# Kernel tuning notes

Hardware: AMD Instinct MI355X
Metric: run time of the kernel (lower is better)

Reference implementation:

```python
import jax, jax.numpy as jnp
import numpy as np

D_MODEL = 2048
N_HEAD = 16
B, T = 2, 2048
D_HEAD = D_MODEL // N_HEAD          # 128
D_Q = D_MODEL // 3                  # 682
D_KV = D_MODEL // 2                 # 1024
D_QK_N = D_HEAD // 2                # 64
D_QK_R = D_HEAD // 2                # 64
LN_EPS = 1e-5


def setup_inputs() -> dict:
    key = jax.random.key(0)
    ks = jax.random.split(key, 8)
    s = 0.02
    return {
        'x': jax.random.normal(ks[0], (B, T, D_MODEL), dtype=jnp.float32),
        'Wdq_w': jax.random.normal(ks[1], (D_Q, D_MODEL), dtype=jnp.float32) * s,
        'Wdq_b': jnp.zeros((D_Q,), jnp.float32),
        'qn_g': jnp.ones((D_Q,), jnp.float32),
        'qn_b': jnp.zeros((D_Q,), jnp.float32),
        'Wuq_w': jax.random.normal(ks[2], (D_MODEL, D_Q), dtype=jnp.float32) * s,
        'Wuq_b': jnp.zeros((D_MODEL,), jnp.float32),
        'Wdkv_w': jax.random.normal(ks[3], (D_KV + D_QK_R, D_MODEL), dtype=jnp.float32) * s,
        'Wdkv_b': jnp.zeros((D_KV + D_QK_R,), jnp.float32),
        'kvn_g': jnp.ones((D_KV,), jnp.float32),
        'kvn_b': jnp.zeros((D_KV,), jnp.float32),
        'Wukv_w': jax.random.normal(ks[4], (D_MODEL + N_HEAD * D_QK_N, D_KV), dtype=jnp.float32) * s,
        'Wukv_b': jnp.zeros((D_MODEL + N_HEAD * D_QK_N,), jnp.float32),
        'Wo_w': jax.random.normal(ks[5], (D_MODEL, D_MODEL), dtype=jnp.float32) * s,
        'Wo_b': jnp.zeros((D_MODEL,), jnp.float32),
    }


def _linear(x, w, b):
    return jnp.einsum('...i,oi->...o', x, w) + b


def _layernorm(x, g, b):
    mu = jnp.mean(x, axis=-1, keepdims=True)
    var = jnp.mean(jnp.square(x - mu), axis=-1, keepdims=True)
    return (x - mu) * jax.lax.rsqrt(var + LN_EPS) * g + b


def _rotary(x):
    # Faithful to source: positions are taken from axis 1 of x (B, A, T, d)
    A, d = x.shape[1], x.shape[-1]
    inv_freq = (1.0 / 10000.0) ** (jnp.arange(0, d, 2, dtype=jnp.float32) / d)
    freqs = jnp.arange(A, dtype=jnp.float32)[:, None] * inv_freq[None, :]
    cos = jnp.cos(freqs)[None, :, None, :]
    sin = jnp.sin(freqs)[None, :, None, :]
    x1, x2 = jnp.split(x, 2, axis=-1)
    return jnp.concatenate([x1 * cos + x2 * sin, -x1 * sin + x2 * cos], axis=-1)


def reference(x, Wdq_w, Wdq_b, qn_g, qn_b, Wuq_w, Wuq_b,
              Wdkv_w, Wdkv_b, kvn_g, kvn_b, Wukv_w, Wukv_b, Wo_w, Wo_b):
    Bx, Tx, C = x.shape
    # Q path: down-proj -> norm -> up-proj
    c_q = _layernorm(_linear(x, Wdq_w, Wdq_b), qn_g, qn_b)
    q = _linear(c_q, Wuq_w, Wuq_b).reshape(Bx, Tx, N_HEAD, D_HEAD).transpose(0, 2, 1, 3)
    q_n, q_r = q[..., :D_QK_N], q[..., D_QK_N:]
    q_r = _rotary(q_r)
    # KV path
    c_kv = _linear(x, Wdkv_w, Wdkv_b)
    kv_n, k_r = c_kv[..., :D_KV], c_kv[..., D_KV:]
    kv_n = _layernorm(kv_n, kvn_g, kvn_b)
    kv = _linear(kv_n, Wukv_w, Wukv_b).reshape(Bx, Tx, N_HEAD, D_HEAD + D_QK_N).transpose(0, 2, 1, 3)
    k_n, v = kv[..., :D_QK_N], kv[..., D_QK_N:]
    k_r = k_r.reshape(Bx, Tx, 1, D_QK_R).transpose(0, 2, 1, 3)  # (B,1,T,dr)
    k_r = _rotary(k_r)  # identity here (single position), kept for fidelity
    k_r = jnp.broadcast_to(k_r, (Bx, N_HEAD, Tx, D_QK_R))
    q_full = jnp.concatenate([q_n, q_r], axis=-1)   # (B,H,T,d_head)
    k_full = jnp.concatenate([k_n, k_r], axis=-1)   # (B,H,T,d_head)
    # causal SDPA (scale = 1/sqrt(q dim))
    scale = 1.0 / np.sqrt(D_HEAD)
    scores = jnp.einsum('bhqd,bhkd->bhqk', q_full, k_full) * scale
    causal = jnp.tril(jnp.ones((Tx, Tx), dtype=bool))
    scores = jnp.where(causal[None, None], scores, jnp.finfo(scores.dtype).min)
    p = jax.nn.softmax(scores, axis=-1)
    y = jnp.einsum('bhqk,bhkd->bhqd', p, v)
    y = y.transpose(0, 2, 1, 3).reshape(Bx, Tx, C)
    return _linear(y, Wo_w, Wo_b)
```

## Files before the change

### kernel.cpp

```cpp
#include <hip/hip_runtime.h>
#include <math.h>

#define TOK 4096
#define DM 2048
#define DQ 682
#define DQP 704
#define DKV 1024
#define DUKV 3072
#define NH 16
#define T_SEQ 2048
#define NQKV 1792

typedef __attribute__((ext_vector_type(8))) short short8;
typedef __attribute__((ext_vector_type(4))) float floatx4;
typedef __attribute__((ext_vector_type(2))) unsigned int uint2v;

__device__ __forceinline__ unsigned short f2bf(float f) {
  union { float f; unsigned int u; } v; v.f = f;
  unsigned int u = v.u;
  u += 0x7fffu + ((u >> 16) & 1u);
  return (unsigned short)(u >> 16);
}
__device__ __forceinline__ unsigned short f2bf_fast(float f) {
  union { float f; unsigned int u; } v; v.f = f;
  return (unsigned short)((v.u + 0x8000u) >> 16);
}

typedef __attribute__((address_space(1))) const unsigned int as1_u32;
typedef __attribute__((address_space(3))) unsigned int as3_u32;
__device__ __forceinline__ void async16(const void* g, void* l) {
  __builtin_amdgcn_global_load_lds((as1_u32*)g, (as3_u32*)l, 16, 0, 0);
}

__global__ __launch_bounds__(256) void gemm_bf16_db(
    const unsigned short* __restrict__ A, int lda,
    const unsigned short* __restrict__ B, int ldb,
    const float* __restrict__ bias, float* __restrict__ C, int ldc,
    int Nvalid, int K)
{
  __shared__ __align__(16) unsigned short sm[16384];
  const int tid = threadIdx.x;
  const int w = tid >> 6;
  const int lane = tid & 63;
  const int q = lane >> 4;
  const int r = lane & 15;
  const int bm = blockIdx.y * 128;
  const int bn = blockIdx.x * 128;

  floatx4 acc[4][4];
#pragma unroll
  for (int i = 0; i < 4; i++)
#pragma unroll
    for (int j = 0; j < 4; j++) acc[i][j] = (floatx4){0.f, 0.f, 0.f, 0.f};

  const int srow = tid >> 2;
  const int scol = (tid & 3) * 8;
  const unsigned short* Ag0 = A + (size_t)(bm + srow) * lda + scol;
  const unsigned short* Ag1 = A + (size_t)(bm + 64 + srow) * lda + scol;
  const unsigned short* Bg0 = B + (size_t)(bn + srow) * ldb + scol;
  const unsigned short* Bg1 = B + (size_t)(bn + 64 + srow) * ldb + scol;

  const int mrow0 = (w >> 1) * 64;
  const int ncol0 = (w & 1) * 64;

  async16(Ag0, &sm[w * 512]);
  async16(Ag1, &sm[2048 + w * 512]);
  async16(Bg0, &sm[8192 + w * 512]);
  async16(Bg1, &sm[8192 + 2048 + w * 512]);

  for (int k0 = 0; k0 < K; k0 += 32) {
    const int cur = (k0 >> 5) & 1;
    __syncthreads();
    if (k0 + 32 < K) {
      const int nxt = cur ^ 1;
      async16(Ag0 + k0 + 32, &sm[nxt * 4096 + w * 512]);
      async16(Ag1 + k0 + 32, &sm[nxt * 4096 + 2048 + w * 512]);
      async16(Bg0 + k0 + 32, &sm[8192 + nxt * 4096 + w * 512]);
      async16(Bg1 + k0 + 32, &sm[8192 + nxt * 4096 + 2048 + w * 512]);
    }
    const unsigned short* As = &sm[cur * 4096];
    const unsigned short* Bs = &sm[8192 + cur * 4096];
    short8 a[4], b[4];
#pragma unroll
    for (int i = 0; i < 4; i++)
      a[i] = *(const short8*)&As[(mrow0 + i * 16 + r) * 32 + q * 8];
#pragma unroll
    for (int j = 0; j < 4; j++)
      b[j] = *(const short8*)&Bs[(ncol0 + j * 16 + r) * 32 + q * 8];
#pragma unroll
    for (int i = 0; i < 4; i++)
#pragma unroll
      for (int j = 0; j < 4; j++)
        acc[i][j] = __builtin_amdgcn_mfma_f32_16x16x32_bf16(a[i], b[j], acc[i][j], 0, 0, 0);
  }

#pragma unroll
  for (int j = 0; j < 4; j++) {
    int gc = bn + ncol0 + j * 16 + r;
    if (gc >= Nvalid) continue;
    float bv = bias[gc];
#pragma unroll
    for (int i = 0; i < 4; i++) {
#pragma unroll
      for (int v = 0; v < 4; v++) {
        int gr = bm + mrow0 + i * 16 + q * 4 + v;
        C[(size_t)gr * ldc + gc] = acc[i][j][v] + bv;
      }
    }
  }
}

__global__ __launch_bounds__(256) void gemm_up_fused(
    const unsigned short* __restrict__ Aq, const unsigned short* __restrict__ Bq,
    const float* __restrict__ biasq, unsigned short* __restrict__ Qall,
    const unsigned short* __restrict__ Akv, const unsigned short* __restrict__ Bkv,
    const float* __restrict__ biaskv, unsigned short* __restrict__ kvout)
{
  __shared__ __align__(16) unsigned short sm[16384];
  const int tid = threadIdx.x;
  const int w = tid >> 6;
  const int lane = tid & 63;
  const int q = lane >> 4;
  const int r = lane & 15;
  const int bx = blockIdx.x;
  const bool isQ = bx < 16;
  const int bn = isQ ? bx * 128 : (bx - 16) * 128;
  const int bm = blockIdx.y * 128;
  const int K = isQ ? DQP : DKV;
  const unsigned short* A = isQ ? Aq : Akv;
  const unsigned short* B = isQ ? Bq : Bkv;

  floatx4 acc[4][4];
#pragma unroll
  for (int i = 0; i < 4; i++)
#pragma unroll
    for (int j = 0; j < 4; j++) acc[i][j] = (floatx4){0.f, 0.f, 0.f, 0.f};

  const int srow = tid >> 2;
  const int scol = (tid & 3) * 8;
  const unsigned short* Ag0 = A + (size_t)(bm + srow) * K + scol;
  const unsigned short* Ag1 = A + (size_t)(bm + 64 + srow) * K + scol;
  const unsigned short* Bg0 = B + (size_t)(bn + srow) * K + scol;
  const unsigned short* Bg1 = B + (size_t)(bn + 64 + srow) * K + scol;

  const int mrow0 = (w >> 1) * 64;
  const int ncol0 = (w & 1) * 64;

  async16(Ag0, &sm[w * 512]);
  async16(Ag1, &sm[2048 + w * 512]);
  async16(Bg0, &sm[8192 + w * 512]);
  async16(Bg1, &sm[8192 + 2048 + w * 512]);

  for (int k0 = 0; k0 < K; k0 += 32) {
    const int cur = (k0 >> 5) & 1;
    __syncthreads();
    if (k0 + 32 < K) {
      const int nxt = cur ^ 1;
      async16(Ag0 + k0 + 32, &sm[nxt * 4096 + w * 512]);
      async16(Ag1 + k0 + 32, &sm[nxt * 4096 + 2048 + w * 512]);
      async16(Bg0 + k0 + 32, &sm[8192 + nxt * 4096 + w * 512]);
      async16(Bg1 + k0 + 32, &sm[8192 + nxt * 4096 + 2048 + w * 512]);
    }
    const unsigned short* As = &sm[cur * 4096];
    const unsigned short* Bs = &sm[8192 + cur * 4096];
    short8 a[4], b[4];
#pragma unroll
    for (int i = 0; i < 4; i++)
      a[i] = *(const short8*)&As[(mrow0 + i * 16 + r) * 32 + q * 8];
#pragma unroll
    for (int j = 0; j < 4; j++)
      b[j] = *(const short8*)&Bs[(ncol0 + j * 16 + r) * 32 + q * 8];
#pragma unroll
    for (int i = 0; i < 4; i++)
#pragma unroll
      for (int j = 0; j < 4; j++)
        acc[i][j] = __builtin_amdgcn_mfma_f32_16x16x32_bf16(a[i], b[j], acc[i][j], 0, 0, 0);
  }

  if (!isQ) {
#pragma unroll
    for (int j = 0; j < 4; j++) {
      int gc = bn + ncol0 + j * 16 + r;
      float bv = biaskv[gc];
#pragma unroll
      for (int i = 0; i < 4; i++) {
#pragma unroll
        for (int v = 0; v < 4; v++) {
          int gr = bm + mrow0 + i * 16 + q * 4 + v;
          kvout[(size_t)gr * DUKV + gc] = f2bf(acc[i][j][v] + bv);
        }
      }
    }
    return;
  }

  const int h = bx;
  const float QS = (float)(0.08838834764831845 * 1.4426950408889634);
  if ((w & 1) == 0) {
#pragma unroll
    for (int j = 0; j < 4; j++) {
      int d = j * 16 + r;
      float bv = biasq[h * 128 + d];
#pragma unroll
      for (int i = 0; i < 4; i++) {
#pragma unroll
        for (int v = 0; v < 4; v++) {
          int gr = bm + mrow0 + i * 16 + q * 4 + v;
          int bb = gr >> 11, t = gr & 2047;
          Qall[(((size_t)(bb * NH + h)) * T_SEQ + t) * 128 + d] =
              f2bf((acc[i][j][v] + bv) * QS);
        }
      }
    }
  } else {
    float cs[2], sn[2], bv1[2], bv2[2];
#pragma unroll
    for (int jp = 0; jp < 2; jp++) {
      int jj = jp * 16 + r;
      float ang = (float)h * exp2f(-(float)jj * (13.287712379549449f / 32.0f));
      cs[jp] = cosf(ang); sn[jp] = sinf(ang);
      bv1[jp] = biasq[h * 128 + 64 + jj];
      bv2[jp] = biasq[h * 128 + 96 + jj];
    }
#pragma unroll
    for (int i = 0; i < 4; i++) {
#pragma unroll
      for (int v = 0; v < 4; v++) {
        int gr = bm + mrow0 + i * 16 + q * 4 + v;
        int bb = gr >> 11, t = gr & 2047;
        unsigned short* Qr = Qall + (((size_t)(bb * NH + h)) * T_SEQ + t) * 128;
#pragma unroll
        for (int jp = 0; jp < 2; jp++) {
          int jj = jp * 16 + r;
          float x1 = acc[i][jp][v] + bv1[jp];
          float x2 = acc[i][jp + 2][v] + bv2[jp];
          Qr[64 + jj] = f2bf((x1 * cs[jp] + x2 * sn[jp]) * QS);
          Qr[96 + jj] = f2bf((x2 * cs[jp] - x1 * sn[jp]) * QS);
        }
      }
    }
  }
}

__global__ __launch_bounds__(256) void cvt_bf16_pad(
    const float* __restrict__ in, unsigned short* __restrict__ out,
    int irows, int icols, int ocols, long total)
{
  long idx = (long)blockIdx.x * 256 + threadIdx.x;
  if (idx >= total) return;
  int rr = (int)(idx / ocols);
  int cc = (int)(idx - (long)rr * ocols);
  out[idx] = (rr < irows && cc < icols) ? f2bf(in[(size_t)rr * icols + cc]) : 0;
}

__device__ __forceinline__ void cvt_region(
    const float* __restrict__ in, unsigned short* __restrict__ out,
    int irows, int icols, int ocols, long idx)
{
  int rr = (int)(idx / ocols);
  int cc = (int)(idx - (long)rr * ocols);
  out[idx] = (rr < irows && cc < icols) ? f2bf(in[(size_t)rr * icols + cc]) : 0;
}

__global__ __launch_bounds__(256) void prep_weights(
    const float* __restrict__ Wdq_w, const float* __restrict__ Wdkv_w,
    const float* __restrict__ Wuq_w, const float* __restrict__ Wukv_w,
    const float* __restrict__ Wo_w,
    const float* __restrict__ Wdq_b, const float* __restrict__ Wdkv_b,
    unsigned short* __restrict__ Wqkv_bf, unsigned short* __restrict__ Wuq_bf,
    unsigned short* __restrict__ Wukv_bf, unsigned short* __restrict__ Wo_bf,
    float* __restrict__ bias_qkv)
{
  const long bx = blockIdx.x;
  if (bx < 5632) {
    cvt_region(Wdq_w, Wqkv_bf, 682, 2048, 2048, bx * 256 + threadIdx.x);
  } else if (bx < 14336) {
    cvt_region(Wdkv_w, Wqkv_bf + 704L * 2048, 1088, 2048, 2048,
               (bx - 5632) * 256 + threadIdx.x);
  } else if (bx < 19968) {
    cvt_region(Wuq_w, Wuq_bf, 2048, 682, 704, (bx - 14336) * 256 + threadIdx.x);
  } else if (bx < 32256) {
    cvt_region(Wukv_w, Wukv_bf, 3072, 1024, 1024, (bx - 19968) * 256 + threadIdx.x);
  } else if (bx < 48640) {
    cvt_region(Wo_w, Wo_bf, 2048, 2048, 2048, (bx - 32256) * 256 + threadIdx.x);
  } else {
    int i = (int)(bx - 48640) * 256 + threadIdx.x;
    if (i < NQKV)
      bias_qkv[i] = (i < DQ) ? Wdq_b[i] : ((i < DQP) ? 0.f : Wdkv_b[i - DQP]);
  }
}

__device__ __forceinline__ float block_sum(float v, float* sbuf) {
#pragma unroll
  for (int off = 32; off > 0; off >>= 1) v += __shfl_down(v, off, 64);
  int wid = threadIdx.x >> 6;
  __syncthreads();
  if ((threadIdx.x & 63) == 0) sbuf[wid] = v;
  __syncthreads();
  return sbuf[0] + sbuf[1] + sbuf[2] + sbuf[3];
}

__global__ __launch_bounds__(256) void ln_bf16_kernel(
    const float* __restrict__ in, int istride,
    unsigned short* __restrict__ out, int ocols,
    const float* __restrict__ g, const float* __restrict__ bta, int D)
{
  __shared__ float sbuf[4];
  size_t row = blockIdx.x;
  const float* xr = in + row * istride;
  float s = 0.f;
  for (int i = threadIdx.x; i < D; i += 256) s += xr[i];
  float mu = block_sum(s, sbuf) / (float)D;
  float v = 0.f;
  for (int i = threadIdx.x; i < D; i += 256) { float d = xr[i] - mu; v += d * d; }
  float var = block_sum(v, sbuf) / (float)D;
  float rstd = rsqrtf(var + 1e-5f);
  unsigned short* orow = out + row * ocols;
  for (int i = threadIdx.x; i < ocols; i += 256)
    orow[i] = (i < D) ? f2bf((xr[i] - mu) * rstd * g[i] + bta[i]) : 0;
}

__global__ __launch_bounds__(256) void repack_k_blk(
    const unsigned short* __restrict__ kv_bf, const float* __restrict__ cqkv,
    unsigned short* __restrict__ K)
{
  int idx = blockIdx.x * 256 + threadIdx.x;
  int dlow = idx & 31;
  int tt   = (idx >> 5) & 63;
  int dhi  = (idx >> 11) & 3;
  int kt   = (idx >> 13) & 31;
  int bh   = idx >> 18;
  int d = dhi * 32 + dlow;
  int t = kt * 64 + tt;
  int b = bh >> 4, h = bh & 15;
  unsigned short val;
  if (d < 64)
    val = kv_bf[((size_t)(b * T_SEQ + t)) * DUKV + h * 192 + d];
  else
    val = f2bf(cqkv[((size_t)(b * T_SEQ + t)) * NQKV + 1728 + (d - 64)]);
  K[idx] = val;
}

__global__ __launch_bounds__(256) void repack_v_blk(
    const unsigned short* __restrict__ kv_bf, unsigned short* __restrict__ V)
{
  __shared__ unsigned short T[64 * 132];
  int kt = blockIdx.x, bh = blockIdx.y;
  int b = bh >> 4, h = bh & 15;
  int tid = threadIdx.x;
#pragma unroll
  for (int p = 0; p < 8; p++) {
    int t = p * 8 + (tid >> 5);
    int dbase = (tid & 31) * 4;
    const unsigned short* src =
        kv_bf + ((size_t)(b * T_SEQ + kt * 64 + t)) * DUKV + h * 192 + 64 + dbase;
    unsigned short v0 = src[0], v1 = src[1], v2 = src[2], v3 = src[3];
    unsigned short* dst = &T[t * 132 + dbase];
    dst[0] = v0; dst[1] = v1; dst[2] = v2; dst[3] = v3;
  }
  __syncthreads();
  unsigned short* out = V + ((size_t)(bh * 32 + kt)) * 8192;
#pragma unroll
  for (int p = 0; p < 4; p++) {
    int o = p * 2048 + tid * 8;
    int c2 = o >> 12;
    int dd = (o >> 5) & 127;
    int tl = o & 31;
    short8 pack;
#pragma unroll
    for (int i = 0; i < 8; i++)
      pack[i] = (short)T[(c2 * 32 + tl + i) * 132 + dd];
    *(short8*)&out[o] = pack;
  }
}

__global__ __launch_bounds__(256, 2) void attn_mfma3(
    const unsigned short* __restrict__ Qall,
    const unsigned short* __restrict__ Kblk,
    const unsigned short* __restrict__ Vblk,
    unsigned short* __restrict__ y)
{
  __shared__ __align__(16) unsigned short sm[37376];
  const int x = (int)blockIdx.x;
  const int b = (int)blockIdx.z;
  const int qt = b ? (15 - x) : x;
  const int h = blockIdx.y;
  const int tid = threadIdx.x;
  const int w = tid >> 6, lane = tid & 63, q = lane >> 4, r = lane & 15;
  const int bh = b * NH + h;

  short8 qb[2][4];
#pragma unroll
  for (int g = 0; g < 2; g++) {
    const unsigned short* Qrow =
        Qall + ((size_t)bh * T_SEQ + (size_t)qt * 128 + w * 32 + g * 16 + r) * 128 + q * 8;
#pragma unroll
    for (int c = 0; c < 4; c++) qb[g][c] = *(const short8*)(Qrow + c * 32);
  }

  floatx4 oacc[2][8];
#pragma unroll
  for (int g = 0; g < 2; g++)
#pragma unroll
    for (int jd = 0; jd < 8; jd++) oacc[g][jd] = (floatx4){0.f, 0.f, 0.f, 0.f};
  float m_i[2] = {-3.0e38f, -3.0e38f}, l_i[2] = {0.f, 0.f};

  const char* Kg0 = (const char*)(Kblk + ((size_t)(bh * 32)) * 8192);
  const char* Vg0 = (const char*)(Vblk + ((size_t)(bh * 32)) * 8192);
  char* smB = (char*)sm;
  unsigned short* Psw = sm + 32768 + w * 1152;
  const int ktmax = 2 * qt + 1;

#pragma unroll
  for (int i = 0; i < 4; i++) {
    async16(Kg0 + i * 4096 + w * 1024 + lane * 16, smB + i * 4096 + w * 1024);
    async16(Vg0 + i * 4096 + w * 1024 + lane * 16, smB + 32768 + i * 4096 + w * 1024);
  }

  for (int kt = 0; kt <= ktmax; kt++) {
    const int cur = kt & 1;
    __syncthreads();
    if (kt < ktmax) {
      const int nxt = cur ^ 1;
      const char* Kg = Kg0 + (size_t)(kt + 1) * 16384;
      const char* Vg = Vg0 + (size_t)(kt + 1) * 16384;
#pragma unroll
      for (int i = 0; i < 4; i++) {
        async16(Kg + i * 4096 + w * 1024 + lane * 16,
                smB + nxt * 16384 + i * 4096 + w * 1024);
        async16(Vg + i * 4096 + w * 1024 + lane * 16,
                smB + 32768 + nxt * 16384 + i * 4096 + w * 1024);
      }
    }

    const bool activeW = (kt * 64 <= qt * 128 + w * 32 + 31);
    if (activeW) {
      const unsigned short* KsC = sm + cur * 8192;
      const unsigned short* VsC = sm + 16384 + cur * 8192;

      floatx4 sacc[2][4];
#pragma unroll
      for (int g = 0; g < 2; g++)
#pragma unroll
        for (int j = 0; j < 4; j++) sacc[g][j] = (floatx4){0.f, 0.f, 0.f, 0.f};
#pragma unroll
      for (int c = 0; c < 4; c++) {
        short8 ak[4];
#pragma unroll
        for (int j = 0; j < 4; j++)
          ak[j] = *(const short8*)&KsC[c * 2048 + (j * 16 + r) * 32 + q * 8];
#pragma unroll
        for (int g = 0; g < 2; g++)
#pragma unroll
          for (int j = 0; j < 4; j++)
            sacc[g][j] = __builtin_amdgcn_mfma_f32_16x16x32_bf16(ak[j], qb[g][c], sacc[g][j], 0, 0, 0);
      }

#pragma unroll
      for (int g = 0; g < 2; g++) {
        float sv[16];
#pragma unroll
        for (int j = 0; j < 4; j++)
#pragma unroll
          for (int v = 0; v < 4; v++) sv[j * 4 + v] = sacc[g][j][v];
        const int rel = qt * 128 + w * 32 + g * 16 + r - kt * 64;
        if (rel < 63) {
#pragma unroll
          for (int j = 0; j < 4; j++)
#pragma unroll
            for (int v = 0; v < 4; v++)
              if (j * 16 + q * 4 + v > rel) sv[j * 4 + v] = -3.0e38f;
        }
        float rm = sv[0];
#pragma unroll
        for (int t16 = 1; t16 < 16; t16++) rm = fmaxf(rm, sv[t16]);
        rm = fmaxf(rm, __shfl_xor(rm, 16, 64));
        rm = fmaxf(rm, __shfl_xor(rm, 32, 64));
        float mnew = fmaxf(m_i[g], rm);
        float alpha = exp2f(m_i[g] - mnew);
        m_i[g] = mnew;
        float p[16], rsum = 0.f;
#pragma unroll
        for (int t16 = 0; t16 < 16; t16++) { p[t16] = exp2f(sv[t16] - mnew); rsum += p[t16]; }
        rsum += __shfl_xor(rsum, 16, 64);
        rsum += __shfl_xor(rsum, 32, 64);
        l_i[g] = l_i[g] * alpha + rsum;
#pragma unroll
        for (int jd = 0; jd < 8; jd++) {
          oacc[g][jd][0] *= alpha; oacc[g][jd][1] *= alpha;
          oacc[g][jd][2] *= alpha; oacc[g][jd][3] *= alpha;
        }
#pragma unroll
        for (int j = 0; j < 4; j++) {
          unsigned int lo = (unsigned int)f2bf_fast(p[j * 4 + 0]) |
                            ((unsigned int)f2bf_fast(p[j * 4 + 1]) << 16);
          unsigned int hi = (unsigned int)f2bf_fast(p[j * 4 + 2]) |
                            ((unsigned int)f2bf_fast(p[j * 4 + 3]) << 16);
          uint2v pk; pk[0] = lo; pk[1] = hi;
          *(uint2v*)&Psw[r * 72 + j * 16 + q * 4] = pk;
        }
#pragma unroll
        for (int c2 = 0; c2 < 2; c2++) {
          short8 pb = *(const short8*)&Psw[r * 72 + c2 * 32 + q * 8];
#pragma unroll
          for (int jd = 0; jd < 8; jd++) {
            short8 bv = *(const short8*)&VsC[c2 * 4096 + (jd * 16 + r) * 32 + q * 8];
            oacc[g][jd] = __builtin_amdgcn_mfma_f32_16x16x32_bf16(bv, pb, oacc[g][jd], 0, 0, 0);
          }
        }
      }
    }
  }

#pragma unroll
  for (int g = 0; g < 2; g++) {
    float inv = 1.0f / l_i[g];
    unsigned short* yr =
        y + ((size_t)(b * T_SEQ) + (size_t)qt * 128 + w * 32 + g * 16 + r) * DM + h * 128;
#pragma unroll
    for (int jd = 0; jd < 8; jd++) {
      unsigned short o0 = f2bf(oacc[g][jd][0] * inv);
      unsigned short o1 = f2bf(oacc[g][jd][1] * inv);
      unsigned short o2 = f2bf(oacc[g][jd][2] * inv);
      unsigned short o3 = f2bf(oacc[g][jd][3] * inv);
      unsigned int lo = (unsigned int)o0 | ((unsigned int)o1 << 16);
      unsigned int hi = (unsigned int)o2 | ((unsigned int)o3 << 16);
      unsigned int* dst = (unsigned int*)(yr + jd * 16 + q * 4);
      dst[0] = lo; dst[1] = hi;
    }
  }
}

extern "C" void kernel_launch(void* const* d_in, const int* in_sizes, int n_in,
                              void* d_out, int out_size, void* d_ws, size_t ws_size,
                              hipStream_t stream) {
  const float* x      = (const float*)d_in[0];
  const float* Wdq_w  = (const float*)d_in[1];
  const float* Wdq_b  = (const float*)d_in[2];
  const float* qn_g   = (const float*)d_in[3];
  const float* qn_b   = (const float*)d_in[4];
  const float* Wuq_w  = (const float*)d_in[5];
  const float* Wuq_b  = (const float*)d_in[6];
  const float* Wdkv_w = (const float*)d_in[7];
  const float* Wdkv_b = (const float*)d_in[8];
  const float* kvn_g  = (const float*)d_in[9];
  const float* kvn_b  = (const float*)d_in[10];
  const float* Wukv_w = (const float*)d_in[11];
  const float* Wukv_b = (const float*)d_in[12];
  const float* Wo_w   = (const float*)d_in[13];
  const float* Wo_b   = (const float*)d_in[14];
  float* out = (float*)d_out;

  float* ws = (float*)d_ws;
  unsigned short* x_bf    = (unsigned short*)(ws);
  unsigned short* y_bf    = (unsigned short*)(ws);
  unsigned short* Wqkv_bf = (unsigned short*)(ws + 4194304);
  unsigned short* Wuq_bf  = (unsigned short*)(ws + 6029312);
  unsigned short* Wukv_bf = (unsigned short*)(ws + 6750208);
  float* bias_qkv = ws + 8323072;
  float* c_qkv    = ws + 8324864;
  unsigned short* c_q_bf = (unsigned short*)(ws + 15664896);
  unsigned short* kvn_bf = (unsigned short*)(ws + 17106688);
  unsigned short* kv_bf  = (unsigned short*)(ws + 19203840);
  unsigned short* Q_all  = (unsigned short*)(ws + 25495296);
  unsigned short* K_blk  = (unsigned short*)(ws + 29689600);
  unsigned short* V_blk  = (unsigned short*)(ws + 33883904);
  unsigned short* Wo_bf  = (unsigned short*)(ws + 38078208);

  dim3 blk(256);

  cvt_bf16_pad<<<(4096L*2048 + 255) / 256, blk, 0, stream>>>(x, x_bf, 4096, 2048, 2048, 4096L*2048);
  prep_weights<<<48647, blk, 0, stream>>>(Wdq_w, Wdkv_w, Wuq_w, Wukv_w, Wo_w,
                                          Wdq_b, Wdkv_b,
                                          Wqkv_bf, Wuq_bf, Wukv_bf, Wo_bf, bias_qkv);

  gemm_bf16_db<<<dim3(14, 32), blk, 0, stream>>>(x_bf, 2048, Wqkv_bf, 2048, bias_qkv, c_qkv, NQKV, NQKV, 2048);
  ln_bf16_kernel<<<TOK, blk, 0, stream>>>(c_qkv, NQKV, c_q_bf, DQP, qn_g, qn_b, DQ);
  ln_bf16_kernel<<<TOK, blk, 0, stream>>>(c_qkv + DQP, NQKV, kvn_bf, DKV, kvn_g, kvn_b, DKV);
  gemm_up_fused<<<dim3(40, 32), blk, 0, stream>>>(c_q_bf, Wuq_bf, Wuq_b, Q_all,
                                                  kvn_bf, Wukv_bf, Wukv_b, kv_bf);
  repack_k_blk<<<(2 * NH * T_SEQ * 128) / 256, blk, 0, stream>>>(kv_bf, c_qkv, K_blk);
  repack_v_blk<<<dim3(32, 32), blk, 0, stream>>>(kv_bf, V_blk);
  attn_mfma3<<<dim3(16, 16, 2), blk, 0, stream>>>(Q_all, K_blk, V_blk, y_bf);
  gemm_bf16_db<<<dim3(16, 32), blk, 0, stream>>>(y_bf, 2048, Wo_bf, 2048, Wo_b, out, DM, DM, 2048);
}
```

Before: 426.9 us.

## Fuse K/V repacking into GEMM epilogues and share rope keys across heads

The up-projection epilogue now writes K_nope and V straight into the blocked attention layouts, so the kv_bf buffer and the two repack kernels go away. The down-projection GEMM writes the rope key once per batch in blocked bf16 form, and attention loads it from a buffer shared by all heads. The two layernorm launches become one dual kernel, and the attention grid is flattened so causal tiles are scheduled in a new order. The scattered 2-byte epilogue stores are uncoalesced and could cost more than the repack passes they replace.

```diff
diff --git a/kernel.cpp b/kernel.cpp
--- a/kernel.cpp
+++ b/kernel.cpp
@@ -110,11 +110,98 @@
   }
 }
 
+__global__ __launch_bounds__(256) void gemm_dqkv(
+    const unsigned short* __restrict__ A,
+    const unsigned short* __restrict__ B,
+    const float* __restrict__ bias, float* __restrict__ C,
+    unsigned short* __restrict__ Kr)
+{
+  __shared__ __align__(16) unsigned short sm[16384];
+  const int tid = threadIdx.x;
+  const int w = tid >> 6;
+  const int lane = tid & 63;
+  const int q = lane >> 4;
+  const int r = lane & 15;
+  const int bm = blockIdx.y * 128;
+  const int bn = blockIdx.x * 128;
+  const int K = 2048;
+
+  floatx4 acc[4][4];
+#pragma unroll
+  for (int i = 0; i < 4; i++)
+#pragma unroll
+    for (int j = 0; j < 4; j++) acc[i][j] = (floatx4){0.f, 0.f, 0.f, 0.f};
+
+  const int srow = tid >> 2;
+  const int scol = (tid & 3) * 8;
+  const unsigned short* Ag0 = A + (size_t)(bm + srow) * K + scol;
+  const unsigned short* Ag1 = A + (size_t)(bm + 64 + srow) * K + scol;
+  const unsigned short* Bg0 = B + (size_t)(bn + srow) * K + scol;
+  const unsigned short* Bg1 = B + (size_t)(bn + 64 + srow) * K + scol;
+
+  const int mrow0 = (w >> 1) * 64;
+  const int ncol0 = (w & 1) * 64;
+
+  async16(Ag0, &sm[w * 512]);
+  async16(Ag1, &sm[2048 + w * 512]);
+  async16(Bg0, &sm[8192 + w * 512]);
+  async16(Bg1, &sm[8192 + 2048 + w * 512]);
+
+  for (int k0 = 0; k0 < K; k0 += 32) {
+    const int cur = (k0 >> 5) & 1;
+    __syncthreads();
+    if (k0 + 32 < K) {
+      const int nxt = cur ^ 1;
+      async16(Ag0 + k0 + 32, &sm[nxt * 4096 + w * 512]);
+      async16(Ag1 + k0 + 32, &sm[nxt * 4096 + 2048 + w * 512]);
+      async16(Bg0 + k0 + 32, &sm[8192 + nxt * 4096 + w * 512]);
+      async16(Bg1 + k0 + 32, &sm[8192 + nxt * 4096 + 2048 + w * 512]);
+    }
+    const unsigned short* As = &sm[cur * 4096];
+    const unsigned short* Bs = &sm[8192 + cur * 4096];
+    short8 a[4], b[4];
+#pragma unroll
+    for (int i = 0; i < 4; i++)
+      a[i] = *(const short8*)&As[(mrow0 + i * 16 + r) * 32 + q * 8];
+#pragma unroll
+    for (int j = 0; j < 4; j++)
+      b[j] = *(const short8*)&Bs[(ncol0 + j * 16 + r) * 32 + q * 8];
+#pragma unroll
+    for (int i = 0; i < 4; i++)
+#pragma unroll
+      for (int j = 0; j < 4; j++)
+        acc[i][j] = __builtin_amdgcn_mfma_f32_16x16x32_bf16(a[i], b[j], acc[i][j], 0, 0, 0);
+  }
+
+#pragma unroll
+  for (int j = 0; j < 4; j++) {
+    int gc = bn + ncol0 + j * 16 + r;
+    float bv = bias[gc];
+    const bool rope = (gc >= 1728);
+    const int dr = gc - 1728;
+#pragma unroll
+    for (int i = 0; i < 4; i++) {
+#pragma unroll
+      for (int v = 0; v < 4; v++) {
+        int gr = bm + mrow0 + i * 16 + q * 4 + v;
+        float val = acc[i][j][v] + bv;
+        C[(size_t)gr * NQKV + gc] = val;
+        if (rope) {
+          int bb = gr >> 11, tt = gr & 2047;
+          Kr[((size_t)(bb * 32 + (tt >> 6))) * 4096 + (dr >> 5) * 2048 +
+             (tt & 63) * 32 + (dr & 31)] = f2bf(val);
+        }
+      }
+    }
+  }
+}
+
 __global__ __launch_bounds__(256) void gemm_up_fused(
     const unsigned short* __restrict__ Aq, const unsigned short* __restrict__ Bq,
     const float* __restrict__ biasq, unsigned short* __restrict__ Qall,
     const unsigned short* __restrict__ Akv, const unsigned short* __restrict__ Bkv,
-    const float* __restrict__ biaskv, unsigned short* __restrict__ kvout)
+    const float* __restrict__ biaskv,
+    unsigned short* __restrict__ Kn, unsigned short* __restrict__ Vb)
 {
   __shared__ __align__(16) unsigned short sm[16384];
   const int tid = threadIdx.x;
@@ -182,12 +269,25 @@
     for (int j = 0; j < 4; j++) {
       int gc = bn + ncol0 + j * 16 + r;
       float bv = biaskv[gc];
+      int hh = gc / 192;
+      int rel = gc - hh * 192;
 #pragma unroll
       for (int i = 0; i < 4; i++) {
 #pragma unroll
         for (int v = 0; v < 4; v++) {
           int gr = bm + mrow0 + i * 16 + q * 4 + v;
-          kvout[(size_t)gr * DUKV + gc] = f2bf(acc[i][j][v] + bv);
+          int bb = gr >> 11, tt = gr & 2047;
+          int bhh = bb * NH + hh;
+          int kt = tt >> 6;
+          unsigned short val = f2bf(acc[i][j][v] + bv);
+          if (rel < 64) {
+            Kn[((size_t)(bhh * 32 + kt)) * 4096 + (rel >> 5) * 2048 +
+               (tt & 63) * 32 + (rel & 31)] = val;
+          } else {
+            int d = rel - 64;
+            Vb[((size_t)(bhh * 32 + kt)) * 8192 + ((tt >> 5) & 1) * 4096 +
+               d * 32 + (tt & 31)] = val;
+          }
         }
       }
     }
@@ -300,14 +400,23 @@
   return sbuf[0] + sbuf[1] + sbuf[2] + sbuf[3];
 }
 
-__global__ __launch_bounds__(256) void ln_bf16_kernel(
-    const float* __restrict__ in, int istride,
-    unsigned short* __restrict__ out, int ocols,
-    const float* __restrict__ g, const float* __restrict__ bta, int D)
+__global__ __launch_bounds__(256) void ln_dual(
+    const float* __restrict__ cqkv,
+    unsigned short* __restrict__ outq, unsigned short* __restrict__ outkv,
+    const float* __restrict__ qg, const float* __restrict__ qb,
+    const float* __restrict__ kg, const float* __restrict__ kb)
 {
   __shared__ float sbuf[4];
-  size_t row = blockIdx.x;
-  const float* xr = in + row * istride;
+  const int row = blockIdx.x;
+  const bool isQ = row < 4096;
+  const int r2 = isQ ? row : row - 4096;
+  const float* xr = cqkv + (size_t)r2 * NQKV + (isQ ? 0 : DQP);
+  const int D = isQ ? DQ : DKV;
+  const int ocols = isQ ? DQP : DKV;
+  const float* g = isQ ? qg : kg;
+  const float* bta = isQ ? qb : kb;
+  unsigned short* orow = (isQ ? outq : outkv) + (size_t)r2 * ocols;
+
   float s = 0.f;
   for (int i = threadIdx.x; i < D; i += 256) s += xr[i];
   float mu = block_sum(s, sbuf) / (float)D;
@@ -315,79 +424,26 @@
   for (int i = threadIdx.x; i < D; i += 256) { float d = xr[i] - mu; v += d * d; }
   float var = block_sum(v, sbuf) / (float)D;
   float rstd = rsqrtf(var + 1e-5f);
-  unsigned short* orow = out + row * ocols;
   for (int i = threadIdx.x; i < ocols; i += 256)
     orow[i] = (i < D) ? f2bf((xr[i] - mu) * rstd * g[i] + bta[i]) : 0;
 }
 
-__global__ __launch_bounds__(256) void repack_k_blk(
-    const unsigned short* __restrict__ kv_bf, const float* __restrict__ cqkv,
-    unsigned short* __restrict__ K)
-{
-  int idx = blockIdx.x * 256 + threadIdx.x;
-  int dlow = idx & 31;
-  int tt   = (idx >> 5) & 63;
-  int dhi  = (idx >> 11) & 3;
-  int kt   = (idx >> 13) & 31;
-  int bh   = idx >> 18;
-  int d = dhi * 32 + dlow;
-  int t = kt * 64 + tt;
-  int b = bh >> 4, h = bh & 15;
-  unsigned short val;
-  if (d < 64)
-    val = kv_bf[((size_t)(b * T_SEQ + t)) * DUKV + h * 192 + d];
-  else
-    val = f2bf(cqkv[((size_t)(b * T_SEQ + t)) * NQKV + 1728 + (d - 64)]);
-  K[idx] = val;
-}
-
-__global__ __launch_bounds__(256) void repack_v_blk(
-    const unsigned short* __restrict__ kv_bf, unsigned short* __restrict__ V)
-{
-  __shared__ unsigned short T[64 * 132];
-  int kt = blockIdx.x, bh = blockIdx.y;
-  int b = bh >> 4, h = bh & 15;
-  int tid = threadIdx.x;
-#pragma unroll
-  for (int p = 0; p < 8; p++) {
-    int t = p * 8 + (tid >> 5);
-    int dbase = (tid & 31) * 4;
-    const unsigned short* src =
-        kv_bf + ((size_t)(b * T_SEQ + kt * 64 + t)) * DUKV + h * 192 + 64 + dbase;
-    unsigned short v0 = src[0], v1 = src[1], v2 = src[2], v3 = src[3];
-    unsigned short* dst = &T[t * 132 + dbase];
-    dst[0] = v0; dst[1] = v1; dst[2] = v2; dst[3] = v3;
-  }
-  __syncthreads();
-  unsigned short* out = V + ((size_t)(bh * 32 + kt)) * 8192;
-#pragma unroll
-  for (int p = 0; p < 4; p++) {
-    int o = p * 2048 + tid * 8;
-    int c2 = o >> 12;
-    int dd = (o >> 5) & 127;
-    int tl = o & 31;
-    short8 pack;
-#pragma unroll
-    for (int i = 0; i < 8; i++)
-      pack[i] = (short)T[(c2 * 32 + tl + i) * 132 + dd];
-    *(short8*)&out[o] = pack;
-  }
-}
-
-__global__ __launch_bounds__(256, 2) void attn_mfma3(
+__global__ __launch_bounds__(256, 2) void attn_mfma4(
     const unsigned short* __restrict__ Qall,
-    const unsigned short* __restrict__ Kblk,
-    const unsigned short* __restrict__ Vblk,
+    const unsigned short* __restrict__ Kn,
+    const unsigned short* __restrict__ Kr,
+    const unsigned short* __restrict__ Vb,
     unsigned short* __restrict__ y)
 {
   __shared__ __align__(16) unsigned short sm[37376];
-  const int x = (int)blockIdx.x;
-  const int b = (int)blockIdx.z;
-  const int qt = b ? (15 - x) : x;
-  const int h = blockIdx.y;
+  const int id = (int)blockIdx.x;
+  const int bhid = id & 31;
+  const int xx = id >> 5;
+  const int qt = (xx < 8) ? xx : (23 - xx);
+  const int h = bhid & 15, b = bhid >> 4;
   const int tid = threadIdx.x;
   const int w = tid >> 6, lane = tid & 63, q = lane >> 4, r = lane & 15;
-  const int bh = b * NH + h;
+  const int bh = bhid;
 
   short8 qb[2][4];
 #pragma unroll
@@ -405,32 +461,40 @@
     for (int jd = 0; jd < 8; jd++) oacc[g][jd] = (floatx4){0.f, 0.f, 0.f, 0.f};
   float m_i[2] = {-3.0e38f, -3.0e38f}, l_i[2] = {0.f, 0.f};
 
-  const char* Kg0 = (const char*)(Kblk + ((size_t)(bh * 32)) * 8192);
-  const char* Vg0 = (const char*)(Vblk + ((size_t)(bh * 32)) * 8192);
+  const char* KnG = (const char*)(Kn + (size_t)bh * 32 * 4096);
+  const char* KrG = (const char*)(Kr + (size_t)b * 32 * 4096);
+  const char* VG  = (const char*)(Vb + (size_t)bh * 32 * 8192);
   char* smB = (char*)sm;
   unsigned short* Psw = sm + 32768 + w * 1152;
   const int ktmax = 2 * qt + 1;
 
 #pragma unroll
-  for (int i = 0; i < 4; i++) {
-    async16(Kg0 + i * 4096 + w * 1024 + lane * 16, smB + i * 4096 + w * 1024);
-    async16(Vg0 + i * 4096 + w * 1024 + lane * 16, smB + 32768 + i * 4096 + w * 1024);
-  }
+  for (int i = 0; i < 2; i++) {
+    async16(KnG + i * 4096 + w * 1024 + lane * 16, smB + i * 4096 + w * 1024);
+    async16(KrG + i * 4096 + w * 1024 + lane * 16, smB + 8192 + i * 4096 + w * 1024);
+  }
+#pragma unroll
+  for (int i = 0; i < 4; i++)
+    async16(VG + i * 4096 + w * 1024 + lane * 16, smB + 32768 + i * 4096 + w * 1024);
 
   for (int kt = 0; kt <= ktmax; kt++) {
     const int cur = kt & 1;
     __syncthreads();
     if (kt < ktmax) {
       const int nxt = cur ^ 1;
-      const char* Kg = Kg0 + (size_t)(kt + 1) * 16384;
-      const char* Vg = Vg0 + (size_t)(kt + 1) * 16384;
-#pragma unroll
-      for (int i = 0; i < 4; i++) {
-        async16(Kg + i * 4096 + w * 1024 + lane * 16,
-                smB + nxt * 16384 + i * 4096 + w * 1024);
-        async16(Vg + i * 4096 + w * 1024 + lane * 16,
-                smB + 32768 + nxt * 16384 + i * 4096 + w * 1024);
-      }
+      const char* kn = KnG + (size_t)(kt + 1) * 8192;
+      const char* kr = KrG + (size_t)(kt + 1) * 8192;
+      const char* vg = VG + (size_t)(kt + 1) * 16384;
+      char* kd = smB + nxt * 16384;
+      char* vd = smB + 32768 + nxt * 16384;
+#pragma unroll
+      for (int i = 0; i < 2; i++) {
+        async16(kn + i * 4096 + w * 1024 + lane * 16, kd + i * 4096 + w * 1024);
+        async16(kr + i * 4096 + w * 1024 + lane * 16, kd + 8192 + i * 4096 + w * 1024);
+      }
+#pragma unroll
+      for (int i = 0; i < 4; i++)
+        async16(vg + i * 4096 + w * 1024 + lane * 16, vd + i * 4096 + w * 1024);
     }
 
     const bool activeW = (kt * 64 <= qt * 128 + w * 32 + 31);
@@ -561,11 +625,11 @@
   float* c_qkv    = ws + 8324864;
   unsigned short* c_q_bf = (unsigned short*)(ws + 15664896);
   unsigned short* kvn_bf = (unsigned short*)(ws + 17106688);
-  unsigned short* kv_bf  = (unsigned short*)(ws + 19203840);
-  unsigned short* Q_all  = (unsigned short*)(ws + 25495296);
-  unsigned short* K_blk  = (unsigned short*)(ws + 29689600);
-  unsigned short* V_blk  = (unsigned short*)(ws + 33883904);
-  unsigned short* Wo_bf  = (unsigned short*)(ws + 38078208);
+  unsigned short* Q_all  = (unsigned short*)(ws + 19203840);
+  unsigned short* Kn_blk = (unsigned short*)(ws + 23398144);
+  unsigned short* Kr_blk = (unsigned short*)(ws + 25495296);
+  unsigned short* V_blk  = (unsigned short*)(ws + 25626368);
+  unsigned short* Wo_bf  = (unsigned short*)(ws + 29820672);
 
   dim3 blk(256);
 
@@ -574,13 +638,11 @@
                                           Wdq_b, Wdkv_b,
                                           Wqkv_bf, Wuq_bf, Wukv_bf, Wo_bf, bias_qkv);
 
-  gemm_bf16_db<<<dim3(14, 32), blk, 0, stream>>>(x_bf, 2048, Wqkv_bf, 2048, bias_qkv, c_qkv, NQKV, NQKV, 2048);
-  ln_bf16_kernel<<<TOK, blk, 0, stream>>>(c_qkv, NQKV, c_q_bf, DQP, qn_g, qn_b, DQ);
-  ln_bf16_kernel<<<TOK, blk, 0, stream>>>(c_qkv + DQP, NQKV, kvn_bf, DKV, kvn_g, kvn_b, DKV);
+  gemm_dqkv<<<dim3(14, 32), blk, 0, stream>>>(x_bf, Wqkv_bf, bias_qkv, c_qkv, Kr_blk);
+  ln_dual<<<8192, blk, 0, stream>>>(c_qkv, c_q_bf, kvn_bf, qn_g, qn_b, kvn_g, kvn_b);
   gemm_up_fused<<<dim3(40, 32), blk, 0, stream>>>(c_q_bf, Wuq_bf, Wuq_b, Q_all,
-                                                  kvn_bf, Wukv_bf, Wukv_b, kv_bf);
-  repack_k_blk<<<(2 * NH * T_SEQ * 128) / 256, blk, 0, stream>>>(kv_bf, c_qkv, K_blk);
-  repack_v_blk<<<dim3(32, 32), blk, 0, stream>>>(kv_bf, V_blk);
-  attn_mfma3<<<dim3(16, 16, 2), blk, 0, stream>>>(Q_all, K_blk, V_blk, y_bf);
+                                                  kvn_bf, Wukv_bf, Wukv_b,
+                                                  Kn_blk, V_blk);
+  attn_mfma4<<<512, blk, 0, stream>>>(Q_all, Kn_blk, Kr_blk, V_blk, y_bf);
   gemm_bf16_db<<<dim3(16, 32), blk, 0, stream>>>(y_bf, 2048, Wo_bf, 2048, Wo_b, out, DM, DM, 2048);
 }
```

Result: no change. 429.4 us (+0.6%).
